# Performance work log

Measured on AMD Instinct MI355X. Metric: run time of the kernel, lower is better.

## Reference

```python
import jax, jax.numpy as jnp
import numpy as np

EPS = 1e-7  # K.epsilon()


def setup_inputs() -> dict:
    key = jax.random.key(0)
    k1, k2, k3 = jax.random.split(key, 3)
    B, T, D = 64, 2048, 256
    x = jax.random.normal(k1, (B, T, D), dtype=jnp.float32)
    W = jax.random.normal(k2, (D, D), dtype=jnp.float32) * (1.0 / np.sqrt(D))
    b = jnp.zeros((D,), dtype=jnp.float32)
    uw = jax.random.normal(k3, (D,), dtype=jnp.float32) * (1.0 / np.sqrt(D))
    mask = jnp.ones((B, T), dtype=jnp.int32)
    return {"x": x, "W": W, "b": b, "uw": uw, "mask": mask}


def reference(x, W, b, uw, mask):
    # x: [B, T, D]; W: [D, D]; b, uw: [D]; mask: [B, T]
    eij = jnp.tanh(jnp.einsum('btd,de->bte', x, W) + b)   # [B, T, D]
    eij = jnp.einsum('btd,d->bt', eij, uw)                # [B, T]
    a = jnp.exp(eij) * mask.astype(x.dtype)               # [B, T]
    a = a / (jnp.sum(a, axis=1, keepdims=True) + EPS)     # normalize over time
    return jnp.einsum('btd,bt->bd', x, a)                 # [B, D]
```

## Files before the change

### kernel.cpp

```cpp
#include <hip/hip_runtime.h>
#include <hip/hip_bf16.h>

#define BB 64
#define TT 2048
#define DD 256
#define EPSF 1e-7f
#define XS_STRIDE 264

typedef __attribute__((ext_vector_type(8))) short v8s;
typedef __attribute__((ext_vector_type(4))) float v4f;

__device__ __forceinline__ float bf2f(unsigned short u) {
    union { unsigned int i; float f; } c;
    c.i = ((unsigned int)u) << 16;
    return c.f;
}

__device__ __forceinline__ unsigned int pack2_bf16(float a, float b) {
    union { __hip_bfloat162 h; unsigned int u; } c;
    c.h = __float22bfloat162_rn(make_float2(a, b));
    return c.u;
}

__device__ __forceinline__ float tanh_fast(float x) {
    float e = __expf(2.0f * x);
    return 1.0f - 2.0f / (e + 1.0f);
}

__global__ __launch_bounds__(256) void pack_wt(const float* __restrict__ W,
                                               unsigned short* __restrict__ Wt) {
    __shared__ float tile[32][33];
    int bx = blockIdx.x & 7;
    int by = blockIdx.x >> 3;
    int r  = threadIdx.x >> 3;
    int c4 = (threadIdx.x & 7) * 4;
    float4 v = *(const float4*)(W + (size_t)(bx * 32 + r) * DD + by * 32 + c4);
    tile[r][c4 + 0] = v.x; tile[r][c4 + 1] = v.y;
    tile[r][c4 + 2] = v.z; tile[r][c4 + 3] = v.w;
    __syncthreads();
    float a0 = tile[c4 + 0][r], a1 = tile[c4 + 1][r];
    float a2 = tile[c4 + 2][r], a3 = tile[c4 + 3][r];
    uint2 pp = make_uint2(pack2_bf16(a0, a1), pack2_bf16(a2, a3));
    *(uint2*)(Wt + (size_t)(by * 32 + r) * DD + bx * 32 + c4) = pp;
}

__global__ __launch_bounds__(256, 3) void fused_att3(const float* __restrict__ x,
                                                     const unsigned short* __restrict__ Wt,
                                                     const float* __restrict__ bias,
                                                     const float* __restrict__ uw,
                                                     const int* __restrict__ mask,
                                                     float* __restrict__ numpart,
                                                     float* __restrict__ denpart) {
    __shared__ unsigned short xs[64 * XS_STRIDE];
    __shared__ float ered[4][64];
    __shared__ float red[4][DD];
    __shared__ float denred[4];

    const int tid  = threadIdx.x;
    const int w    = tid >> 6;
    const int lane = tid & 63;
    const int quad = lane >> 4;
    const int m    = lane & 15;
    const long R0  = (long)blockIdx.x * 64 + w * 16;

    float bias_r[4], uw_r[4];
#pragma unroll
    for (int i = 0; i < 4; ++i) {
        int n = (w * 4 + i) * 16 + m;
        bias_r[i] = bias[n];
        uw_r[i]   = uw[n];
    }

    {
        const float* gp = x + R0 * DD + lane * 4;
        unsigned short* sp = xs + (size_t)(w * 16) * XS_STRIDE + lane * 4;
#pragma unroll 8
        for (int r = 0; r < 16; ++r) {
            float4 v = *(const float4*)(gp + (size_t)r * DD);
            uint2 pp = make_uint2(pack2_bf16(v.x, v.y), pack2_bf16(v.z, v.w));
            *(uint2*)(sp + (size_t)r * XS_STRIDE) = pp;
        }
    }
    __syncthreads();

    float esum[4][4];
#pragma unroll
    for (int mt = 0; mt < 4; ++mt)
#pragma unroll
        for (int r = 0; r < 4; ++r) esum[mt][r] = 0.f;

#pragma unroll
    for (int h = 0; h < 2; ++h) {
        v8s a0[8], a1[8];
        {
            const unsigned short* ap0 = xs + (size_t)(2 * h * 16 + m) * XS_STRIDE + quad * 8;
#pragma unroll
            for (int ks = 0; ks < 8; ++ks) {
                a0[ks] = *(const v8s*)(ap0 + ks * 32);
                a1[ks] = *(const v8s*)(ap0 + 16 * XS_STRIDE + ks * 32);
            }
        }
        v8s bbuf[2][8];
        {
            const unsigned short* bp = Wt + (size_t)(w * 4 * 16 + m) * DD + quad * 8;
#pragma unroll
            for (int ks = 0; ks < 8; ++ks) bbuf[0][ks] = *(const v8s*)(bp + ks * 32);
        }
#pragma unroll
        for (int i = 0; i < 4; ++i) {
            const int cur = i & 1;
            if (i < 3) {
                const unsigned short* bp = Wt + (size_t)((w * 4 + i + 1) * 16 + m) * DD + quad * 8;
#pragma unroll
                for (int ks = 0; ks < 8; ++ks) bbuf[cur ^ 1][ks] = *(const v8s*)(bp + ks * 32);
            }
            v4f acc0 = {0.f, 0.f, 0.f, 0.f};
            v4f acc1 = {0.f, 0.f, 0.f, 0.f};
#pragma unroll
            for (int ks = 0; ks < 8; ++ks) {
                acc0 = __builtin_amdgcn_mfma_f32_16x16x32_bf16(a0[ks], bbuf[cur][ks], acc0, 0, 0, 0);
                acc1 = __builtin_amdgcn_mfma_f32_16x16x32_bf16(a1[ks], bbuf[cur][ks], acc1, 0, 0, 0);
            }
#pragma unroll
            for (int r = 0; r < 4; ++r) {
                esum[2 * h][r]     += tanh_fast(acc0[r] + bias_r[i]) * uw_r[i];
                esum[2 * h + 1][r] += tanh_fast(acc1[r] + bias_r[i]) * uw_r[i];
            }
        }
    }

#pragma unroll
    for (int o = 1; o < 16; o <<= 1)
#pragma unroll
        for (int mt = 0; mt < 4; ++mt)
#pragma unroll
            for (int r = 0; r < 4; ++r)
                esum[mt][r] += __shfl_xor(esum[mt][r], o, 64);
    if (m == 0) {
#pragma unroll
        for (int mt = 0; mt < 4; ++mt)
#pragma unroll
            for (int r = 0; r < 4; ++r)
                ered[w][mt * 16 + quad * 4 + r] = esum[mt][r];
    }
    __syncthreads();

    const int rl = lane & 15;
    float et = ered[0][w * 16 + rl] + ered[1][w * 16 + rl]
             + ered[2][w * 16 + rl] + ered[3][w * 16 + rl];
    float p_loc = __expf(et) * (float)mask[R0 + rl];
    float p_all[16];
#pragma unroll
    for (int t = 0; t < 16; ++t) p_all[t] = __shfl(p_loc, t, 64);
    float den = 0.f;
#pragma unroll
    for (int t = 0; t < 16; ++t) den += p_all[t];

    float num[4] = {0.f, 0.f, 0.f, 0.f};
    {
        const unsigned short* xp = xs + (size_t)(w * 16) * XS_STRIDE + lane * 4;
#pragma unroll
        for (int t = 0; t < 16; ++t) {
            uint2 xv = *(const uint2*)(xp + (size_t)t * XS_STRIDE);
            float pt = p_all[t];
            num[0] += pt * bf2f((unsigned short)(xv.x & 0xffffu));
            num[1] += pt * bf2f((unsigned short)(xv.x >> 16));
            num[2] += pt * bf2f((unsigned short)(xv.y & 0xffffu));
            num[3] += pt * bf2f((unsigned short)(xv.y >> 16));
        }
    }

    *(float4*)&red[w][lane * 4] = make_float4(num[0], num[1], num[2], num[3]);
    if (lane == 0) denred[w] = den;
    __syncthreads();
    float s = red[0][tid] + red[1][tid] + red[2][tid] + red[3][tid];
    numpart[(size_t)blockIdx.x * DD + tid] = s;
    if (tid == 0) denpart[blockIdx.x] = denred[0] + denred[1] + denred[2] + denred[3];
}

__global__ __launch_bounds__(256) void finalize(const float* __restrict__ numpart,
                                                const float* __restrict__ denpart,
                                                float* __restrict__ out) {
    __shared__ float dsh;
    int b = blockIdx.x, d = threadIdx.x;
    if (d == 0) {
        float s = 0.f;
        for (int c = 0; c < 32; ++c) s += denpart[b * 32 + c];
        dsh = s + EPSF;
    }
    __syncthreads();
    float s = 0.f;
#pragma unroll
    for (int c = 0; c < 32; ++c) s += numpart[(size_t)(b * 32 + c) * DD + d];
    out[(size_t)b * DD + d] = s / dsh;
}

extern "C" void kernel_launch(void* const* d_in, const int* in_sizes, int n_in,
                              void* d_out, int out_size, void* d_ws, size_t ws_size,
                              hipStream_t stream) {
    const float* x    = (const float*)d_in[0];
    const float* W    = (const float*)d_in[1];
    const float* bias = (const float*)d_in[2];
    const float* uw   = (const float*)d_in[3];
    const int*   mask = (const int*)d_in[4];
    float*       out  = (float*)d_out;

    char* ws = (char*)d_ws;
    unsigned short* Wt = (unsigned short*)ws;
    float* numpart     = (float*)(ws + 131072);
    float* denpart     = (float*)(ws + 131072 + 2097152);

    pack_wt<<<dim3(64), dim3(256), 0, stream>>>(W, Wt);
    fused_att3<<<dim3(2048), dim3(256), 0, stream>>>(x, Wt, bias, uw, mask, numpart, denpart);
    finalize<<<dim3(64), dim3(256), 0, stream>>>(numpart, denpart, out);
}
```

Measured before the change: 231.6 us.

## Split rows across waves and stage W tiles through LDS with register prefetch

Reorganizes the fused attention kernel so each of two waves owns 32 time rows across all 256 output columns, instead of four waves splitting the column dimension. W^T is streamed in 32-column chunks through shared memory with register double-buffering, replacing per-wave direct global fragment loads. This removes the cross-wave energy reduction in shared memory and lets softmax weights be computed directly from MFMA outputs. The cost is two block barriers per chunk and a smaller block (128 threads) with lower occupancy bounds.

Result: slower. 282.1 us (+21.8%).

```diff
diff --git a/kernel.cpp b/kernel.cpp
--- a/kernel.cpp
+++ b/kernel.cpp
@@ -5,7 +5,7 @@
 #define TT 2048
 #define DD 256
 #define EPSF 1e-7f
-#define XS_STRIDE 264
+#define PADS 272
 
 typedef __attribute__((ext_vector_type(8))) short v8s;
 typedef __attribute__((ext_vector_type(4))) float v4f;
@@ -44,124 +44,130 @@
     *(uint2*)(Wt + (size_t)(by * 32 + r) * DD + bx * 32 + c4) = pp;
 }
 
-__global__ __launch_bounds__(256, 3) void fused_att3(const float* __restrict__ x,
+__global__ __launch_bounds__(128, 2) void fused_att4(const float* __restrict__ x,
                                                      const unsigned short* __restrict__ Wt,
                                                      const float* __restrict__ bias,
                                                      const float* __restrict__ uw,
                                                      const int* __restrict__ mask,
                                                      float* __restrict__ numpart,
                                                      float* __restrict__ denpart) {
-    __shared__ unsigned short xs[64 * XS_STRIDE];
-    __shared__ float ered[4][64];
-    __shared__ float red[4][DD];
-    __shared__ float denred[4];
+    __shared__ __align__(16) unsigned short xbuf[64 * PADS];
+    __shared__ __align__(16) unsigned short bbuf[32 * PADS];
 
     const int tid  = threadIdx.x;
     const int w    = tid >> 6;
     const int lane = tid & 63;
-    const int quad = lane >> 4;
+    const int q    = lane >> 4;
     const int m    = lane & 15;
-    const long R0  = (long)blockIdx.x * 64 + w * 16;
-
-    float bias_r[4], uw_r[4];
-#pragma unroll
-    for (int i = 0; i < 4; ++i) {
-        int n = (w * 4 + i) * 16 + m;
-        bias_r[i] = bias[n];
-        uw_r[i]   = uw[n];
-    }
+    const long RW  = (long)blockIdx.x * 64 + w * 32;
 
     {
-        const float* gp = x + R0 * DD + lane * 4;
-        unsigned short* sp = xs + (size_t)(w * 16) * XS_STRIDE + lane * 4;
+        const float* gp = x + RW * DD + lane * 4;
+        unsigned short* sp = xbuf + (size_t)(w * 32) * PADS + lane * 4;
 #pragma unroll 8
-        for (int r = 0; r < 16; ++r) {
+        for (int r = 0; r < 32; ++r) {
             float4 v = *(const float4*)(gp + (size_t)r * DD);
             uint2 pp = make_uint2(pack2_bf16(v.x, v.y), pack2_bf16(v.z, v.w));
-            *(uint2*)(sp + (size_t)r * XS_STRIDE) = pp;
-        }
-    }
-    __syncthreads();
-
-    float esum[4][4];
-#pragma unroll
-    for (int mt = 0; mt < 4; ++mt)
-#pragma unroll
-        for (int r = 0; r < 4; ++r) esum[mt][r] = 0.f;
-
-#pragma unroll
-    for (int h = 0; h < 2; ++h) {
-        v8s a0[8], a1[8];
+            *(uint2*)(sp + (size_t)r * PADS) = pp;
+        }
+    }
+
+    v8s A[2][8];
+#pragma unroll
+    for (int mt = 0; mt < 2; ++mt) {
+        const unsigned short* ap = xbuf + (size_t)(w * 32 + mt * 16 + m) * PADS + q * 8;
+#pragma unroll
+        for (int ks = 0; ks < 8; ++ks) A[mt][ks] = *(const v8s*)(ap + ks * 32);
+    }
+
+    const int nloc = w * 16 + (lane >> 5);
+    const int c8   = (lane & 31) * 8;
+    uint4 breg[8];
+    {
+        const unsigned short* gB = Wt + (size_t)nloc * DD + c8;
+#pragma unroll
+        for (int it = 0; it < 8; ++it) breg[it] = *(const uint4*)(gB + (size_t)(it * 2) * DD);
+    }
+
+    float esum[2][4] = {{0.f, 0.f, 0.f, 0.f}, {0.f, 0.f, 0.f, 0.f}};
+
+    for (int j = 0; j < 8; ++j) {
+        __syncthreads();
         {
-            const unsigned short* ap0 = xs + (size_t)(2 * h * 16 + m) * XS_STRIDE + quad * 8;
+            unsigned short* sb = bbuf + (size_t)nloc * PADS + c8;
+#pragma unroll
+            for (int it = 0; it < 8; ++it)
+                *(uint4*)(sb + (size_t)(it * 2) * PADS) = breg[it];
+        }
+        if (j < 7) {
+            const unsigned short* gB = Wt + (size_t)((j + 1) * 32 + nloc) * DD + c8;
+#pragma unroll
+            for (int it = 0; it < 8; ++it)
+                breg[it] = *(const uint4*)(gB + (size_t)(it * 2) * DD);
+        }
+        __syncthreads();
+
+        float b_r[2], u_r[2];
+#pragma unroll
+        for (int ntl = 0; ntl < 2; ++ntl) {
+            int n = j * 32 + ntl * 16 + m;
+            b_r[ntl] = bias[n];
+            u_r[ntl] = uw[n];
+        }
+#pragma unroll
+        for (int ntl = 0; ntl < 2; ++ntl) {
+            const unsigned short* bp = bbuf + (size_t)(ntl * 16 + m) * PADS + q * 8;
+            v8s B0[8];
+#pragma unroll
+            for (int ks = 0; ks < 8; ++ks) B0[ks] = *(const v8s*)(bp + ks * 32);
+            v4f a0 = {0.f, 0.f, 0.f, 0.f};
+            v4f a1 = {0.f, 0.f, 0.f, 0.f};
 #pragma unroll
             for (int ks = 0; ks < 8; ++ks) {
-                a0[ks] = *(const v8s*)(ap0 + ks * 32);
-                a1[ks] = *(const v8s*)(ap0 + 16 * XS_STRIDE + ks * 32);
+                a0 = __builtin_amdgcn_mfma_f32_16x16x32_bf16(A[0][ks], B0[ks], a0, 0, 0, 0);
+                a1 = __builtin_amdgcn_mfma_f32_16x16x32_bf16(A[1][ks], B0[ks], a1, 0, 0, 0);
             }
-        }
-        v8s bbuf[2][8];
-        {
-            const unsigned short* bp = Wt + (size_t)(w * 4 * 16 + m) * DD + quad * 8;
-#pragma unroll
-            for (int ks = 0; ks < 8; ++ks) bbuf[0][ks] = *(const v8s*)(bp + ks * 32);
-        }
-#pragma unroll
-        for (int i = 0; i < 4; ++i) {
-            const int cur = i & 1;
-            if (i < 3) {
-                const unsigned short* bp = Wt + (size_t)((w * 4 + i + 1) * 16 + m) * DD + quad * 8;
-#pragma unroll
-                for (int ks = 0; ks < 8; ++ks) bbuf[cur ^ 1][ks] = *(const v8s*)(bp + ks * 32);
+#pragma unroll
+            for (int r = 0; r < 4; ++r) {
+                esum[0][r] += tanh_fast(a0[r] + b_r[ntl]) * u_r[ntl];
+                esum[1][r] += tanh_fast(a1[r] + b_r[ntl]) * u_r[ntl];
             }
-            v4f acc0 = {0.f, 0.f, 0.f, 0.f};
-            v4f acc1 = {0.f, 0.f, 0.f, 0.f};
-#pragma unroll
-            for (int ks = 0; ks < 8; ++ks) {
-                acc0 = __builtin_amdgcn_mfma_f32_16x16x32_bf16(a0[ks], bbuf[cur][ks], acc0, 0, 0, 0);
-                acc1 = __builtin_amdgcn_mfma_f32_16x16x32_bf16(a1[ks], bbuf[cur][ks], acc1, 0, 0, 0);
-            }
-#pragma unroll
-            for (int r = 0; r < 4; ++r) {
-                esum[2 * h][r]     += tanh_fast(acc0[r] + bias_r[i]) * uw_r[i];
-                esum[2 * h + 1][r] += tanh_fast(acc1[r] + bias_r[i]) * uw_r[i];
-            }
-        }
-    }
+        }
+    }
+    __syncthreads();
 
 #pragma unroll
     for (int o = 1; o < 16; o <<= 1)
 #pragma unroll
-        for (int mt = 0; mt < 4; ++mt)
+        for (int mt = 0; mt < 2; ++mt)
 #pragma unroll
             for (int r = 0; r < 4; ++r)
                 esum[mt][r] += __shfl_xor(esum[mt][r], o, 64);
-    if (m == 0) {
-#pragma unroll
-        for (int mt = 0; mt < 4; ++mt)
-#pragma unroll
-            for (int r = 0; r < 4; ++r)
-                ered[w][mt * 16 + quad * 4 + r] = esum[mt][r];
-    }
-    __syncthreads();
-
-    const int rl = lane & 15;
-    float et = ered[0][w * 16 + rl] + ered[1][w * 16 + rl]
-             + ered[2][w * 16 + rl] + ered[3][w * 16 + rl];
-    float p_loc = __expf(et) * (float)mask[R0 + rl];
-    float p_all[16];
-#pragma unroll
-    for (int t = 0; t < 16; ++t) p_all[t] = __shfl(p_loc, t, 64);
+
+    float p_loc[2][4];
+#pragma unroll
+    for (int mt = 0; mt < 2; ++mt) {
+        const int4 mv = *(const int4*)(mask + RW + mt * 16 + q * 4);
+        p_loc[mt][0] = __expf(esum[mt][0]) * (float)mv.x;
+        p_loc[mt][1] = __expf(esum[mt][1]) * (float)mv.y;
+        p_loc[mt][2] = __expf(esum[mt][2]) * (float)mv.z;
+        p_loc[mt][3] = __expf(esum[mt][3]) * (float)mv.w;
+    }
+
+    float p_all[32];
     float den = 0.f;
 #pragma unroll
-    for (int t = 0; t < 16; ++t) den += p_all[t];
+    for (int i = 0; i < 32; ++i) {
+        p_all[i] = __shfl(p_loc[i >> 4][i & 3], ((i >> 2) & 3) * 16 + m, 64);
+        den += p_all[i];
+    }
 
     float num[4] = {0.f, 0.f, 0.f, 0.f};
     {
-        const unsigned short* xp = xs + (size_t)(w * 16) * XS_STRIDE + lane * 4;
-#pragma unroll
-        for (int t = 0; t < 16; ++t) {
-            uint2 xv = *(const uint2*)(xp + (size_t)t * XS_STRIDE);
+        const unsigned short* xp = xbuf + (size_t)(w * 32) * PADS + lane * 4;
+#pragma unroll 8
+        for (int t = 0; t < 32; ++t) {
+            uint2 xv = *(const uint2*)(xp + (size_t)t * PADS);
             float pt = p_all[t];
             num[0] += pt * bf2f((unsigned short)(xv.x & 0xffffu));
             num[1] += pt * bf2f((unsigned short)(xv.x >> 16));
@@ -170,12 +176,13 @@
         }
     }
 
-    *(float4*)&red[w][lane * 4] = make_float4(num[0], num[1], num[2], num[3]);
-    if (lane == 0) denred[w] = den;
-    __syncthreads();
-    float s = red[0][tid] + red[1][tid] + red[2][tid] + red[3][tid];
-    numpart[(size_t)blockIdx.x * DD + tid] = s;
-    if (tid == 0) denpart[blockIdx.x] = denred[0] + denred[1] + denred[2] + denred[3];
+    float* red = (float*)bbuf;
+    *(float4*)&red[w * 256 + lane * 4] = make_float4(num[0], num[1], num[2], num[3]);
+    if (lane == 0) red[512 + w] = den;
+    __syncthreads();
+    numpart[(size_t)blockIdx.x * DD + tid]       = red[tid] + red[256 + tid];
+    numpart[(size_t)blockIdx.x * DD + 128 + tid] = red[128 + tid] + red[384 + tid];
+    if (tid == 0) denpart[blockIdx.x] = red[512] + red[513];
 }
 
 __global__ __launch_bounds__(256) void finalize(const float* __restrict__ numpart,
@@ -211,6 +218,6 @@
     float* denpart     = (float*)(ws + 131072 + 2097152);
 
     pack_wt<<<dim3(64), dim3(256), 0, stream>>>(W, Wt);
-    fused_att3<<<dim3(2048), dim3(256), 0, stream>>>(x, Wt, bias, uw, mask, numpart, denpart);
+    fused_att4<<<dim3(2048), dim3(128), 0, stream>>>(x, Wt, bias, uw, mask, numpart, denpart);
     finalize<<<dim3(64), dim3(256), 0, stream>>>(numpart, denpart, out);
 }
```
